# Kernel tuning notes

Measured on AMD Instinct MI355X. Metric: run time of the kernel, lower is better.

The kernel has to match this reference:

```python
import jax, jax.numpy as jnp
import numpy as np

NH = 12  # num_heads


def setup_inputs() -> dict:
    key = jax.random.key(0)
    k1, k2, k3 = jax.random.split(key, 3)
    B, Hs, Ws, C = 8, 56, 56, 768
    N = Hs * Ws + 1  # +1 cls token
    x = jax.random.normal(k1, (B, N, C), jnp.float32)
    W_qkv = jax.random.normal(k2, (C, 3 * C), jnp.float32) * 0.02  # qkv_bias=False
    W_proj = jax.random.normal(k3, (C, C), jnp.float32) * 0.02
    b_proj = jnp.zeros((C,), jnp.float32)
    return {"x": x, "W_qkv": W_qkv, "W_proj": W_proj, "b_proj": b_proj}


def _criss_cross(x, W_qkv, W_proj, b_proj):
    B, N, C = x.shape
    H = W = int(np.sqrt(N))  # N = H*W + 1 (cls token); int(sqrt(3137)) == 56
    hd = C // NH
    scale = hd ** -0.5
    qkv = (x @ W_qkv).reshape(B, N, 3, NH, hd).transpose(2, 0, 3, 1, 4)
    q, k, v = qkv[0], qkv[1], qkv[2]  # (B, NH, N, hd)
    q_cls, k_cls, v_cls = q[:, :, :1], k[:, :, :1], v[:, :, :1]  # (B, NH, 1, hd)

    def grid(t):  # drop cls, view as spatial grid (B, NH, H, W, hd)
        return t[:, :, 1:].reshape(B, NH, H, W, hd)

    def col_view(t, t_cls):  # column (height) axis with cls prepended: (B, W, NH, 1+H, hd)
        tg = jnp.transpose(grid(t), (0, 3, 1, 2, 4))
        cls = jnp.broadcast_to(t_cls[:, None], (B, W, NH, 1, hd))
        return jnp.concatenate([cls, tg], axis=3)

    def row_view(t):  # row (width) axis: (B, H, NH, W, hd)
        return jnp.transpose(grid(t), (0, 2, 1, 3, 4))

    q_h, k_h, v_h = col_view(q, q_cls), col_view(k, k_cls), col_view(v, v_cls)
    q_w, k_w, v_w = row_view(q), row_view(k), row_view(v)

    s_h = jnp.einsum('bwnqd,bwnkd->bwnqk', q_h, k_h) * scale  # (B, W, NH, 1+H, 1+H)
    s_h = jnp.transpose(s_h, (0, 3, 2, 1, 4))[:, 1:]          # (B, H, NH, W, 1+H)
    s_w = jnp.einsum('bhnqd,bhnkd->bhnqk', q_w, k_w) * scale  # (B, H, NH, W, W)
    s_w = jnp.where(jnp.eye(W, dtype=bool), -jnp.inf, s_w)    # mask self in row attention

    # joint softmax over concatenated column+row scores
    attn = jax.nn.softmax(jnp.concatenate([s_h, s_w], axis=-1), axis=-1)
    a_h, a_w = attn[..., :1 + H], attn[..., 1 + H:]
    a_h = jnp.transpose(a_h, (0, 3, 2, 1, 4))  # (B, W, NH, H, 1+H)

    x_h = jnp.einsum('bwnqk,bwnkd->bqwnd', a_h, v_h).reshape(B, H, W, C)
    x_w = jnp.einsum('bhnqk,bhnkd->bhqnd', a_w, v_w).reshape(B, H, W, C)
    out = (x_h + x_w).reshape(B, H * W, C)

    # cls token attends over the full sequence (including itself)
    s_cls = jnp.einsum('bnqd,bnkd->bnqk', q_cls, k) * scale  # (B, NH, 1, N)
    a_cls = jax.nn.softmax(s_cls, axis=-1)
    x_cls = jnp.einsum('bnqk,bnkd->bqnd', a_cls, v).reshape(B, 1, C)

    out = jnp.concatenate([x_cls, out], axis=1)  # (B, N, C)
    return out @ W_proj + b_proj


def reference(x, W_qkv, W_proj, b_proj):
    return _criss_cross(x, W_qkv, W_proj, b_proj)
```

## Files before the change

### kernel.cpp

```cpp
#include <hip/hip_runtime.h>
#include <math.h>

#define B_   8
#define Hs   56
#define Ws   56
#define Cc   768
#define NHh  12
#define HDd  64
#define Nt   3137
#define HW_  3136
#define C3   2304
#define SCALE 0.125f
#define Mrows (B_ * Nt)
#define Mpad  (99 * 256)

typedef _Float16 half8  __attribute__((ext_vector_type(8)));
typedef _Float16 half4  __attribute__((ext_vector_type(4)));
typedef _Float16 half2_ __attribute__((ext_vector_type(2)));
typedef float floatx4 __attribute__((ext_vector_type(4)));

#define WAITV(N) asm volatile("s_waitcnt vmcnt(" #N ")" ::: "memory")
#define WAITL    asm volatile("s_waitcnt lgkmcnt(0)" ::: "memory")

__device__ __forceinline__ void barrier_mem() {
    asm volatile("" ::: "memory");
    __builtin_amdgcn_s_barrier();
    asm volatile("" ::: "memory");
}

__device__ __forceinline__ void gload_lds16(const _Float16* g, _Float16* l) {
    __builtin_amdgcn_global_load_lds(
        (const __attribute__((address_space(1))) void*)g,
        (__attribute__((address_space(3))) void*)l, 16, 0, 0);
}

__device__ _Float16 g_qkvh[(size_t)Mrows * C3];
__device__ float    g_Ocol[(size_t)B_ * NHh * HW_ * HDd];
__device__ float    g_mcol[(size_t)B_ * NHh * HW_];
__device__ float    g_lcol[(size_t)B_ * NHh * HW_];
__device__ _Float16 g_xh[(size_t)Mpad * Cc];
__device__ _Float16 g_attH[(size_t)Mpad * Cc];
__device__ _Float16 g_WqkvT[(size_t)C3 * Cc];
__device__ _Float16 g_WprojT[(size_t)Cc * Cc];
__device__ float    g_clsP[(size_t)B_ * NHh * 4 * 66];

__global__ __launch_bounds__(256) void cvt_f16(
    const float* __restrict__ in, _Float16* __restrict__ out, int n4)
{
    for (int i = blockIdx.x * 256 + threadIdx.x; i < n4; i += gridDim.x * 256) {
        float4 v = ((const float4*)in)[i];
        half4 h = { (_Float16)v.x, (_Float16)v.y, (_Float16)v.z, (_Float16)v.w };
        ((half4*)out)[i] = h;
    }
}

__global__ __launch_bounds__(256) void transpose_f16(
    const float* __restrict__ in, _Float16* __restrict__ out, int R, int Cq)
{
    __shared__ float t[32][33];
    const int c0 = blockIdx.x * 32, r0 = blockIdx.y * 32;
    const int tx = threadIdx.x & 31, ty = threadIdx.x >> 5;
#pragma unroll
    for (int i = 0; i < 32; i += 8)
        t[ty + i][tx] = in[(size_t)(r0 + ty + i) * Cq + c0 + tx];
    __syncthreads();
#pragma unroll
    for (int i = 0; i < 32; i += 8)
        out[(size_t)(c0 + ty + i) * R + r0 + tx] = (_Float16)t[tx][ty + i];
}

template <typename OutT, int BM>
__global__ __launch_bounds__(512, 2) void gemm_f16(
    const _Float16* __restrict__ A, const _Float16* __restrict__ Bt,
    const float* __restrict__ bias, OutT* __restrict__ Cm,
    int M, int Nd, int K)
{
    constexpr int MI   = BM / 32;
    constexpr int LA   = BM / 128;
    constexpr int ASZh = BM * 32;
    constexpr int BSZh = 256 * 32;
    constexpr int BUFh = ASZh + BSZh;
    constexpr size_t MAINB = (size_t)4 * BUFh * 2;
    constexpr size_t EPIB  = sizeof(OutT) == 2 ? (size_t)BM * 280 * 2
                                               : (size_t)BM * 140 * 4;
    constexpr size_t SMEMB = MAINB > EPIB ? MAINB : EPIB;
    __shared__ __align__(16) char smem[SMEMB];

    const int tid = threadIdx.x;
    const int wave = tid >> 6, lane = tid & 63;
    const int wm = wave & 1, wn = wave >> 1;

    const int bid = blockIdx.y * gridDim.x + blockIdx.x;
    const int perPanel = gridDim.x * 16;
    const int panel = bid / perPanel;
    const int rowsIn = min(16, (int)gridDim.y - panel * 16);
    const int rem = bid - panel * perPanel;
    const int by = panel * 16 + rem % rowsIn;
    const int bx = rem / rowsIn;
    const int mBase = by * BM, nBase = bx * 256;

    const int mU  = ((tid >> 6) << 4) + (tid & 15);
    const int kcU = (tid >> 4) & 3;
    const _Float16* ga = A  + (size_t)(mBase + mU) * K + kcU * 8;
    const _Float16* gb = Bt + (size_t)(nBase + mU) * K + kcU * 8;

    auto stage = [&](int t) {
        char* base = smem + (size_t)(t & 3) * (BUFh * 2);
        _Float16* lA = (_Float16*)base + wave * 512;
        _Float16* lB = (_Float16*)base + ASZh + wave * 512;
        const _Float16* gaK = ga + t * 32;
        const _Float16* gbK = gb + t * 32;
#pragma unroll
        for (int i = 0; i < LA; ++i)
            gload_lds16(gaK + (size_t)i * 128 * K, lA + i * 4096);
#pragma unroll
        for (int i = 0; i < 2; ++i)
            gload_lds16(gbK + (size_t)i * 128 * K, lB + i * 4096);
    };

    const int fo = (lane >> 4) * 128 + (lane & 15) * 8;
    auto readFrags = [&](int t, half8 (&a)[MI], half8 (&b)[4]) {
        const _Float16* bufA = (const _Float16*)(smem + (size_t)(t & 3) * (BUFh * 2));
        const _Float16* bufB = bufA + ASZh;
#pragma unroll
        for (int mi = 0; mi < MI; ++mi)
            a[mi] = *(const half8*)&bufA[(wm * MI + mi) * 512 + fo];
#pragma unroll
        for (int ni = 0; ni < 4; ++ni)
            b[ni] = *(const half8*)&bufB[(wn * 4 + ni) * 512 + fo];
    };

    floatx4 acc[MI][4] = {};
    half8 aX[MI], bX[4], aY[MI], bY[4];

    const int NT = K >> 5;
    stage(0); stage(1); stage(2);
    if constexpr (LA == 2) { WAITV(8); } else { WAITV(6); }
    barrier_mem();
    readFrags(0, aX, bX);

    auto tileBody = [&](int t, half8 (&aC)[MI], half8 (&bC)[4],
                        half8 (&aN)[MI], half8 (&bN)[4]) {
        if (t <= NT - 3) {
            if constexpr (LA == 2) { WAITV(4); } else { WAITV(3); }
        } else {
            WAITV(0);
        }
        barrier_mem();
        if (t + 3 < NT) stage(t + 3);
        __builtin_amdgcn_s_setprio(1);
        if (t + 1 < NT) readFrags(t + 1, aN, bN);
#pragma unroll
        for (int mi = 0; mi < MI; ++mi)
#pragma unroll
            for (int ni = 0; ni < 4; ++ni)
                acc[mi][ni] = __builtin_amdgcn_mfma_f32_16x16x32_f16(
                    bC[ni], aC[mi], acc[mi][ni], 0, 0, 0);
        __builtin_amdgcn_s_setprio(0);
    };

    for (int t = 0; t < NT; t += 2) {
        tileBody(t,     aX, bX, aY, bY);
        tileBody(t + 1, aY, bY, aX, bX);
    }
    WAITL;
    barrier_mem();

    const int mlBase = wm * (BM / 2) + (lane & 15);
    const int nlBase = wn * 64 + ((lane >> 4) << 2);

    if constexpr (sizeof(OutT) == 2) {
        _Float16* Ch = (_Float16*)smem;
#pragma unroll
        for (int ni = 0; ni < 4; ++ni) {
            const int nl = nlBase + ni * 16;
#pragma unroll
            for (int mi = 0; mi < MI; ++mi) {
                const int ml = mlBase + mi * 16;
                floatx4 v = acc[mi][ni];
                half4 h = { (_Float16)v[0], (_Float16)v[1],
                            (_Float16)v[2], (_Float16)v[3] };
                *(half4*)&Ch[ml * 280 + nl] = h;
            }
        }
        barrier_mem();
#pragma unroll
        for (int i = 0; i < BM / 16; ++i) {
            const int f = i * 512 + tid;
            const int row = f >> 5, u = f & 31;
            const int gm = mBase + row;
            if (gm < M)
                *(half8*)&Cm[(size_t)gm * Nd + nBase + u * 8] =
                    *(const half8*)&Ch[row * 280 + u * 8];
        }
    } else {
        float* Cf = (float*)smem;
#pragma unroll
        for (int nh = 0; nh < 2; ++nh) {
            barrier_mem();
            if ((wn >> 1) == nh) {
#pragma unroll
                for (int ni = 0; ni < 4; ++ni) {
                    const int n0 = nBase + wn * 64 + ((lane >> 4) << 2) + ni * 16;
                    float4 bv = bias ? *(const float4*)&bias[n0]
                                     : make_float4(0.f, 0.f, 0.f, 0.f);
                    const int nl = (wn & 1) * 64 + ((lane >> 4) << 2) + ni * 16;
#pragma unroll
                    for (int mi = 0; mi < MI; ++mi) {
                        const int ml = mlBase + mi * 16;
                        floatx4 v = acc[mi][ni];
                        float4 o = make_float4(v[0] + bv.x, v[1] + bv.y,
                                               v[2] + bv.z, v[3] + bv.w);
                        *(float4*)&Cf[ml * 140 + nl] = o;
                    }
                }
            }
            barrier_mem();
#pragma unroll
            for (int i = 0; i < BM / 16; ++i) {
                const int f = i * 512 + tid;
                const int row = f >> 5, u = f & 31;
                const int gm = mBase + row;
                if (gm < M)
                    *(float4*)&Cm[(size_t)gm * Nd + nBase + nh * 128 + u * 4] =
                        *(const float4*)&Cf[row * 140 + u * 4];
            }
        }
    }
}

template <int MODE>
__global__ __launch_bounds__(64) void cc_attn(
    const _Float16* __restrict__ qkvh,
    float* __restrict__ Ocol, float* __restrict__ mcol,
    float* __restrict__ lcol, _Float16* __restrict__ attH)
{
    constexpr int NK = (MODE == 0) ? 57 : 56;
    const int x = blockIdx.x, nh = blockIdx.y, b = blockIdx.z;
    const int lane = threadIdx.x;
    const int q15 = lane & 15, g = lane >> 4;

    __shared__ __align__(16) char smem[18944];
    _Float16* Vt = (_Float16*)smem;
    _Float16* Pl = (_Float16*)(smem + 9216);
    float*    ML = (float*)(smem + 18432);
    float*    Ol = (float*)smem;

    const _Float16* base_b = qkvh + (size_t)(b * Nt) * C3 + nh * HDd;

    auto nrow_k = [&](int key) -> int {
        key = min(key, NK - 1);
        if (MODE == 0) return (key == 0) ? 0 : ((key - 1) * Ws + x + 1);
        return x * Ws + key + 1;
    };
    auto nrow_q = [&](int q) -> int {
        q = min(q, 55);
        return (MODE == 0) ? (q * Ws + x + 1) : (x * Ws + q + 1);
    };

    half8 Kf[4][2], Qf[4][2];
#pragma unroll
    for (int t = 0; t < 4; ++t) {
        const _Float16* kp = base_b + (size_t)nrow_k(t * 16 + q15) * C3 + Cc;
        const _Float16* qp = base_b + (size_t)nrow_q(t * 16 + q15) * C3;
#pragma unroll
        for (int kk = 0; kk < 2; ++kk) {
            Kf[t][kk] = *(const half8*)(kp + kk * 32 + g * 8);
            Qf[t][kk] = *(const half8*)(qp + kk * 32 + g * 8);
        }
    }

#pragma unroll
    for (int it = 0; it < 8; ++it) {
        const int i = it * 64 + lane;
        const int j = i >> 3, c = i & 7;
        half8 v = {};
        if (j < NK)
            v = *(const half8*)(base_b + (size_t)nrow_k(j) * C3 + 2 * Cc + c * 8);
#pragma unroll
        for (int e = 0; e < 8; ++e)
            Vt[(c * 8 + e) * 72 + ((j + 8 * c) & 63)] = v[e];
    }

    floatx4 S[4][4] = {};
#pragma unroll
    for (int kt = 0; kt < 4; ++kt)
#pragma unroll
        for (int qt = 0; qt < 4; ++qt)
#pragma unroll
            for (int kk = 0; kk < 2; ++kk)
                S[kt][qt] = __builtin_amdgcn_mfma_f32_16x16x32_f16(
                    Kf[kt][kk], Qf[qt][kk], S[kt][qt], 0, 0, 0);

    float mq[4], lq[4];
#pragma unroll
    for (int qt = 0; qt < 4; ++qt) {
        const int q = qt * 16 + q15;
        float sv[4][4];
        float mm = -1e30f;
#pragma unroll
        for (int kt = 0; kt < 4; ++kt)
#pragma unroll
            for (int r = 0; r < 4; ++r) {
                const int key = kt * 16 + g * 4 + r;
                float s = S[kt][qt][r] * SCALE;
                const bool bad = (key >= NK) || (MODE == 1 && key == q);
                sv[kt][r] = bad ? -1e30f : s;
                mm = fmaxf(mm, sv[kt][r]);
            }
        mm = fmaxf(mm, __shfl_xor(mm, 16, 64));
        mm = fmaxf(mm, __shfl_xor(mm, 32, 64));
        float ll = 0.f;
#pragma unroll
        for (int kt = 0; kt < 4; ++kt) {
            half4 ph;
#pragma unroll
            for (int r = 0; r < 4; ++r) {
                const float p = __expf(sv[kt][r] - mm);
                ll += p;
                ph[r] = (_Float16)p;
            }
            *(half4*)&Pl[q * 72 + kt * 16 + g * 4] = ph;
        }
        ll += __shfl_xor(ll, 16, 64);
        ll += __shfl_xor(ll, 32, 64);
        mq[qt] = mm; lq[qt] = ll;
    }

    if (g == 0) {
        if (MODE == 0) {
#pragma unroll
            for (int qt = 0; qt < 4; ++qt) {
                const int q = qt * 16 + q15;
                if (q < 56) {
                    const size_t qi = (size_t)((b * NHh + nh) * HW_) + q * Ws + x;
                    mcol[qi] = mq[qt]; lcol[qi] = lq[qt];
                }
            }
        } else {
#pragma unroll
            for (int qt = 0; qt < 4; ++qt) {
                ML[qt * 16 + q15] = mq[qt];
                ML[64 + qt * 16 + q15] = lq[qt];
            }
        }
    }
    __syncthreads();

    half8 Pf[4][2];
#pragma unroll
    for (int qt = 0; qt < 4; ++qt)
#pragma unroll
        for (int kk = 0; kk < 2; ++kk)
            Pf[qt][kk] = *(const half8*)&Pl[(qt * 16 + q15) * 72 + kk * 32 + g * 8];

    floatx4 O[4][4] = {};
#pragma unroll
    for (int dt = 0; dt < 4; ++dt) {
        const int d = dt * 16 + q15;
        const int rot = 8 * (d >> 3);
        half8 Vf0 = *(const half8*)&Vt[d * 72 + ((0 + g * 8 + rot) & 63)];
        half8 Vf1 = *(const half8*)&Vt[d * 72 + ((32 + g * 8 + rot) & 63)];
#pragma unroll
        for (int qt = 0; qt < 4; ++qt) {
            O[dt][qt] = __builtin_amdgcn_mfma_f32_16x16x32_f16(
                Vf0, Pf[qt][0], O[dt][qt], 0, 0, 0);
            O[dt][qt] = __builtin_amdgcn_mfma_f32_16x16x32_f16(
                Vf1, Pf[qt][1], O[dt][qt], 0, 0, 0);
        }
    }
    __syncthreads();

#pragma unroll
    for (int dt = 0; dt < 4; ++dt)
#pragma unroll
        for (int qt = 0; qt < 4; ++qt) {
            float4 f = { O[dt][qt][0], O[dt][qt][1], O[dt][qt][2], O[dt][qt][3] };
            *(float4*)&Ol[(qt * 16 + q15) * 68 + dt * 16 + g * 4] = f;
        }
    __syncthreads();

    const int qq = lane;
    if (qq < 56) {
        if (MODE == 0) {
            const size_t qi = (size_t)((b * NHh + nh) * HW_) + qq * Ws + x;
            float* op = Ocol + qi * HDd;
#pragma unroll
            for (int i = 0; i < 16; ++i)
                *(float4*)(op + i * 4) = *(const float4*)&Ol[qq * 68 + i * 4];
        } else {
            const size_t qi = (size_t)((b * NHh + nh) * HW_) + x * Ws + qq;
            const float mc = mcol[qi], lc = lcol[qi];
            const float mr = ML[qq], lr = ML[64 + qq];
            const float mn = fmaxf(mc, mr);
            const float fc = __expf(mc - mn);
            const float fr = __expf(mr - mn);
            const float inv = 1.f / (lc * fc + lr * fr);
            const int n = x * Ws + qq + 1;
            _Float16* op = attH + (size_t)(b * Nt + n) * Cc + nh * HDd;
            const float* ocp = Ocol + qi * HDd;
#pragma unroll
            for (int i = 0; i < 16; ++i) {
                float4 oc = *(const float4*)(ocp + i * 4);
                const float* oo = &Ol[qq * 68 + i * 4];
                half4 r = { (_Float16)((oc.x * fc + oo[0] * fr) * inv),
                            (_Float16)((oc.y * fc + oo[1] * fr) * inv),
                            (_Float16)((oc.z * fc + oo[2] * fr) * inv),
                            (_Float16)((oc.w * fc + oo[3] * fr) * inv) };
                *(half4*)(op + i * 4) = r;
            }
        }
    }
}

__global__ __launch_bounds__(1024) void cls_part(
    const _Float16* __restrict__ qkvh, float* __restrict__ P)
{
    const int nh = blockIdx.x, b = blockIdx.y, sidx = blockIdx.z;
    const int j0 = sidx * 785, j1 = min(Nt, j0 + 785);
    const int tid = threadIdx.x;
    const int lane = tid & 63, wv = tid >> 6;

    const float qd = (float)qkvh[(size_t)(b * Nt) * C3 + nh * HDd + lane];
    float m = -INFINITY, l = 0.f, Od = 0.f;

    for (int j = j0 + wv; j < j1; j += 16) {
        const _Float16* base = qkvh + (size_t)(b * Nt + j) * C3 + nh * HDd;
        float prod = qd * (float)base[Cc + lane];
#pragma unroll
        for (int off = 32; off >= 1; off >>= 1)
            prod += __shfl_xor(prod, off, 64);
        float s = prod * SCALE;
        float mn = fmaxf(m, s);
        float corr = __expf(m - mn);
        float p = __expf(s - mn);
        l = l * corr + p;
        Od = fmaf(Od, corr, p * (float)base[2 * Cc + lane]);
        m = mn;
    }

    __shared__ float sm[16], sl[16], sO[16][64];
    if (lane == 0) { sm[wv] = m; sl[wv] = l; }
    sO[wv][lane] = Od;
    __syncthreads();

    if (tid < 64) {
        float M2 = sm[0];
#pragma unroll
        for (int i = 1; i < 16; ++i) M2 = fmaxf(M2, sm[i]);
        float L = 0.f, OO = 0.f;
#pragma unroll
        for (int i = 0; i < 16; ++i) {
            float f = __expf(sm[i] - M2);
            L += sl[i] * f;
            OO += sO[i][tid] * f;
        }
        float* pp = P + (size_t)((b * NHh + nh) * 4 + sidx) * 66;
        if (tid == 0) { pp[0] = M2; pp[1] = L; }
        pp[2 + tid] = OO;
    }
}

__global__ __launch_bounds__(64) void cls_merge(
    const float* __restrict__ P, _Float16* __restrict__ attH)
{
    const int nh = blockIdx.x, b = blockIdx.y;
    const int tid = threadIdx.x;
    const float* p0 = P + (size_t)(b * NHh + nh) * 4 * 66;
    float M2 = fmaxf(fmaxf(p0[0], p0[66]), fmaxf(p0[132], p0[198]));
    float L = 0.f, OO = 0.f;
#pragma unroll
    for (int i = 0; i < 4; ++i) {
        const float* pp = p0 + i * 66;
        float f = __expf(pp[0] - M2);
        L += pp[1] * f;
        OO += pp[2 + tid] * f;
    }
    attH[(size_t)(b * Nt) * Cc + nh * HDd + tid] = (_Float16)(OO / L);
}

extern "C" void kernel_launch(void* const* d_in, const int* in_sizes, int n_in,
                              void* d_out, int out_size, void* d_ws, size_t ws_size,
                              hipStream_t stream)
{
    const float* x     = (const float*)d_in[0];
    const float* Wqkv  = (const float*)d_in[1];
    const float* Wproj = (const float*)d_in[2];
    const float* bproj = (const float*)d_in[3];
    float* out = (float*)d_out;

    _Float16* qkvh;   hipGetSymbolAddress((void**)&qkvh,   HIP_SYMBOL(g_qkvh));
    float*    Ocol;   hipGetSymbolAddress((void**)&Ocol,   HIP_SYMBOL(g_Ocol));
    float*    mcol;   hipGetSymbolAddress((void**)&mcol,   HIP_SYMBOL(g_mcol));
    float*    lcol;   hipGetSymbolAddress((void**)&lcol,   HIP_SYMBOL(g_lcol));
    _Float16* xh;     hipGetSymbolAddress((void**)&xh,     HIP_SYMBOL(g_xh));
    _Float16* attH;   hipGetSymbolAddress((void**)&attH,   HIP_SYMBOL(g_attH));
    _Float16* WqkvT;  hipGetSymbolAddress((void**)&WqkvT,  HIP_SYMBOL(g_WqkvT));
    _Float16* WprojT; hipGetSymbolAddress((void**)&WprojT, HIP_SYMBOL(g_WprojT));
    float*    clsP;   hipGetSymbolAddress((void**)&clsP,   HIP_SYMBOL(g_clsP));

    cvt_f16<<<4096, 256, 0, stream>>>(x, xh, (Mrows * Cc) / 4);
    transpose_f16<<<dim3(C3 / 32, Cc / 32), 256, 0, stream>>>(Wqkv, WqkvT, Cc, C3);
    transpose_f16<<<dim3(Cc / 32, Cc / 32), 256, 0, stream>>>(Wproj, WprojT, Cc, Cc);

    gemm_f16<_Float16, 256><<<dim3(C3 / 256, Mpad / 256), 512, 0, stream>>>(
        xh, WqkvT, nullptr, qkvh, Mrows, C3, Cc);

    cc_attn<0><<<dim3(Ws, NHh, B_), 64, 0, stream>>>(qkvh, Ocol, mcol, lcol, attH);
    cls_part<<<dim3(NHh, B_, 4), 1024, 0, stream>>>(qkvh, clsP);
    cls_merge<<<dim3(NHh, B_), 64, 0, stream>>>(clsP, attH);
    cc_attn<1><<<dim3(Hs, NHh, B_), 64, 0, stream>>>(qkvh, Ocol, mcol, lcol, attH);

    gemm_f16<float, 128><<<dim3(Cc / 256, Mpad / 128), 512, 0, stream>>>(
        attH, WprojT, bproj, out, Mrows, Cc, Cc);
}
```

Baseline: 482.7 us.

## Restructure GEMM main loop into ping-pong phases with split A/B staging

Replaces the register double-buffered fragment prefetch with a phased schedule. Each K-tile's LDS fragments are read, the next global-to-LDS loads are issued between phases, and the MFMAs are fenced with sched_barrier and workgroup barriers. For MI==8 the A tile is split into two halves so the B staging overlaps the second half. The aim is to cut register pressure and interleave memory issue with MFMA work, at the cost of extra barriers and lgkmcnt waits per tile that may serialize LDS reads with compute.

```diff
diff --git a/kernel.cpp b/kernel.cpp
--- a/kernel.cpp
+++ b/kernel.cpp
@@ -104,64 +104,81 @@
     const _Float16* ga = A  + (size_t)(mBase + mU) * K + kcU * 8;
     const _Float16* gb = Bt + (size_t)(nBase + mU) * K + kcU * 8;
 
-    auto stage = [&](int t) {
+    auto stageA = [&](int t) {
         char* base = smem + (size_t)(t & 3) * (BUFh * 2);
         _Float16* lA = (_Float16*)base + wave * 512;
-        _Float16* lB = (_Float16*)base + ASZh + wave * 512;
         const _Float16* gaK = ga + t * 32;
-        const _Float16* gbK = gb + t * 32;
 #pragma unroll
         for (int i = 0; i < LA; ++i)
             gload_lds16(gaK + (size_t)i * 128 * K, lA + i * 4096);
+    };
+    auto stageB = [&](int t) {
+        char* base = smem + (size_t)(t & 3) * (BUFh * 2);
+        _Float16* lB = (_Float16*)base + ASZh + wave * 512;
+        const _Float16* gbK = gb + t * 32;
 #pragma unroll
         for (int i = 0; i < 2; ++i)
             gload_lds16(gbK + (size_t)i * 128 * K, lB + i * 4096);
     };
 
     const int fo = (lane >> 4) * 128 + (lane & 15) * 8;
-    auto readFrags = [&](int t, half8 (&a)[MI], half8 (&b)[4]) {
+
+    floatx4 acc[MI][4] = {};
+
+    const int NT = K >> 5;
+    stageA(0); stageB(0); stageA(1); stageB(1); stageA(2); stageB(2);
+
+    for (int t = 0; t < NT; ++t) {
         const _Float16* bufA = (const _Float16*)(smem + (size_t)(t & 3) * (BUFh * 2));
         const _Float16* bufB = bufA + ASZh;
-#pragma unroll
-        for (int mi = 0; mi < MI; ++mi)
-            a[mi] = *(const half8*)&bufA[(wm * MI + mi) * 512 + fo];
+        const bool st = (t + 3 < NT);
+
+        if (t <= NT - 3)      { if constexpr (LA == 2) { WAITV(8); } else { WAITV(6); } }
+        else if (t == NT - 2) { if constexpr (LA == 2) { WAITV(4); } else { WAITV(3); } }
+        else                  { WAITV(0); }
+        barrier_mem();
+
+        half8 b0[4], a0[4];
 #pragma unroll
         for (int ni = 0; ni < 4; ++ni)
-            b[ni] = *(const half8*)&bufB[(wn * 4 + ni) * 512 + fo];
-    };
-
-    floatx4 acc[MI][4] = {};
-    half8 aX[MI], bX[4], aY[MI], bY[4];
-
-    const int NT = K >> 5;
-    stage(0); stage(1); stage(2);
-    if constexpr (LA == 2) { WAITV(8); } else { WAITV(6); }
-    barrier_mem();
-    readFrags(0, aX, bX);
-
-    auto tileBody = [&](int t, half8 (&aC)[MI], half8 (&bC)[4],
-                        half8 (&aN)[MI], half8 (&bN)[4]) {
-        if (t <= NT - 3) {
-            if constexpr (LA == 2) { WAITV(4); } else { WAITV(3); }
-        } else {
-            WAITV(0);
-        }
+            b0[ni] = *(const half8*)&bufB[(wn * 4 + ni) * 512 + fo];
+#pragma unroll
+        for (int mi = 0; mi < 4 && mi < MI; ++mi)
+            a0[mi] = *(const half8*)&bufA[(wm * MI + mi) * 512 + fo];
+        if (st) stageA(t + 3);
+        if constexpr (MI == 4) { if (st) stageB(t + 3); }
         barrier_mem();
-        if (t + 3 < NT) stage(t + 3);
+        WAITL;
+        __builtin_amdgcn_sched_barrier(0);
         __builtin_amdgcn_s_setprio(1);
-        if (t + 1 < NT) readFrags(t + 1, aN, bN);
-#pragma unroll
-        for (int mi = 0; mi < MI; ++mi)
+#pragma unroll
+        for (int mi = 0; mi < 4 && mi < MI; ++mi)
 #pragma unroll
             for (int ni = 0; ni < 4; ++ni)
                 acc[mi][ni] = __builtin_amdgcn_mfma_f32_16x16x32_f16(
-                    bC[ni], aC[mi], acc[mi][ni], 0, 0, 0);
+                    b0[ni], a0[mi], acc[mi][ni], 0, 0, 0);
         __builtin_amdgcn_s_setprio(0);
-    };
-
-    for (int t = 0; t < NT; t += 2) {
-        tileBody(t,     aX, bX, aY, bY);
-        tileBody(t + 1, aY, bY, aX, bX);
+        barrier_mem();
+
+        if constexpr (MI == 8) {
+            half8 a1[4];
+#pragma unroll
+            for (int mi = 0; mi < 4; ++mi)
+                a1[mi] = *(const half8*)&bufA[(wm * MI + 4 + mi) * 512 + fo];
+            if (st) stageB(t + 3);
+            barrier_mem();
+            WAITL;
+            __builtin_amdgcn_sched_barrier(0);
+            __builtin_amdgcn_s_setprio(1);
+#pragma unroll
+            for (int mi = 0; mi < 4; ++mi)
+#pragma unroll
+                for (int ni = 0; ni < 4; ++ni)
+                    acc[4 + mi][ni] = __builtin_amdgcn_mfma_f32_16x16x32_f16(
+                        b0[ni], a1[mi], acc[4 + mi][ni], 0, 0, 0);
+            __builtin_amdgcn_s_setprio(0);
+            barrier_mem();
+        }
     }
     WAITL;
     barrier_mem();
```

New measurement: 504.0 us. 4.4% more time.
